# Optimization experiments

Measured on AMD Instinct MI355X. Metric: run time of the kernel, lower is better.

Reference implementation:

```python
import jax, jax.numpy as jnp
import numpy as np


def setup_inputs() -> dict:
    key = jax.random.key(0)
    k1, k2, k3, k4 = jax.random.split(key, 4)
    N, C_in, C_out, H, W, K = 32, 128, 256, 56, 56, 3
    x = jax.random.normal(k1, (N, C_in, H, W), dtype=jnp.float32)
    # ternary weights in {-1, 0, +1}, stored as int8 like the torch buffer
    w_q = jax.random.randint(k2, (C_out, C_in, K, K), -1, 2).astype(jnp.int8)
    s = jax.random.uniform(k3, (C_out, 1, 1), dtype=jnp.float32) + 0.5
    bias = jax.random.normal(k4, (C_out,), dtype=jnp.float32)
    return {"x": x, "w_q": w_q, "s": s, "bias": bias}


def reference(x, w_q, s, bias):
    # y = conv2d(x, w_q.float()) * s + bias, stride=1, padding=1, dilation=1, groups=1
    w = w_q.astype(x.dtype)  # ternary {-1,0,+1} cast to float, as in torch
    y = jax.lax.conv_general_dilated(
        x, w,
        window_strides=(1, 1),
        padding=((1, 1), (1, 1)),
        lhs_dilation=(1, 1),
        rhs_dilation=(1, 1),
        dimension_numbers=("NCHW", "OIHW", "NCHW"),
        feature_group_count=1,
    )
    y = y * s  # s: [C_out,1,1] broadcasts over [N,C_out,H,W]
    y = y + bias.reshape(1, -1, 1, 1)
    return y
```

## Files before the change

kernel.cpp:

```cpp
#include <hip/hip_runtime.h>
#include <hip/hip_bf16.h>

typedef unsigned short ushort_t;

#define N_IMG 32
#define C_IN  128
#define C_OUT 256
#define H_SZ  56
#define W_SZ  56
#define HW_SZ (H_SZ * W_SZ)
#define K_TOT (C_IN * 9)
#define SP_TOT (N_IMG * HW_SZ)

typedef __attribute__((ext_vector_type(8))) short bf16x8;
typedef __attribute__((ext_vector_type(4))) float floatx4;

__device__ __forceinline__ void gl_lds16(const ushort_t* g, ushort_t* l) {
  __builtin_amdgcn_global_load_lds(
      (const __attribute__((address_space(1))) void*)g,
      (__attribute__((address_space(3))) void*)l, 16, 0, 0);
}

__device__ __forceinline__ ushort_t f2bf(float f) {
  __hip_bfloat16 b = __float2bfloat16(f);
  return *reinterpret_cast<ushort_t*>(&b);
}

__global__ void wtrans_kernel(const int* __restrict__ wq, ushort_t* __restrict__ wt,
                              ushort_t* __restrict__ zeros) {
  int tid = threadIdx.x;
  if (blockIdx.x == 0 && tid < 128) zeros[tid] = 0;
  int idx = blockIdx.x * 256 + tid;
  if (idx >= C_OUT * K_TOT) return;
  int co = idx / K_TOT;
  int k  = idx - co * K_TOT;
  int tap = k >> 7;
  int c   = k & 127;
  int kh = tap / 3, kw = tap - kh * 3;
  int v = wq[((co * C_IN + c) * 3 + kh) * 3 + kw];
  wt[idx] = f2bf((float)v);
}

#define LDT 69
__global__ __launch_bounds__(256) void xtrans_kernel(const float* __restrict__ x,
                                                     ushort_t* __restrict__ xt) {
  __shared__ float tile[64 * LDT];
  int b = blockIdx.x;
  int n = b / 98;
  int r = b - n * 98;
  int cg = r / 49;
  int hwg = r - cg * 49;
  int hw0 = hwg * 64, c0 = cg * 64;
  int t = threadIdx.x;
  int cl = t >> 4;
  int f4 = t & 15;
  const float* xb = x + ((size_t)(n * C_IN + c0) * HW_SZ + hw0);
#pragma unroll
  for (int p = 0; p < 4; ++p) {
    int c = p * 16 + cl;
    float4 v = *(const float4*)(xb + (size_t)c * HW_SZ + f4 * 4);
    float* dst = &tile[c * LDT + f4 * 4];
    dst[0] = v.x; dst[1] = v.y; dst[2] = v.z; dst[3] = v.w;
  }
  __syncthreads();
  int cp  = t & 31;
  int hwl = t >> 5;
  ushort_t* ob = xt + (size_t)(n * HW_SZ + hw0) * C_IN + c0;
#pragma unroll
  for (int p = 0; p < 8; ++p) {
    int hw = p * 8 + hwl;
    unsigned int u = (unsigned int)f2bf(tile[(2 * cp) * LDT + hw]) |
                     ((unsigned int)f2bf(tile[(2 * cp + 1) * LDT + hw]) << 16);
    *(unsigned int*)&ob[(size_t)hw * C_IN + 2 * cp] = u;
  }
}

__global__ __launch_bounds__(256) void bitconv_kernel(
    const ushort_t* __restrict__ wt, const ushort_t* __restrict__ xt,
    const ushort_t* __restrict__ zeros,
    const float* __restrict__ s, const float* __restrict__ bias,
    float* __restrict__ out) {
  __shared__ ushort_t As[128 * 64];
  __shared__ ushort_t Bs[128 * 64];

  int d = blockIdx.x;
  int sp_idx = (d >> 4) * 8 + (d & 7);
  int co0 = ((d >> 3) & 1) * 128;
  int sp0 = sp_idx * 128;

  int tid  = threadIdx.x;
  int lane = tid & 63;
  int wid  = tid >> 6;
  int l15  = lane & 15;
  int quad = lane >> 4;
  int lrow8 = lane >> 3;
  int lk8   = (lane & 7) * 8;
  int wave_m = (wid >> 1) * 64;
  int wave_n = (wid & 1) * 64;

  const ushort_t* a_src0 = wt + (size_t)(co0 + wid * 32 + lrow8) * K_TOT + lk8;
  int bh[4], bw[4];
  const ushort_t* b_img[4];
#pragma unroll
  for (int j = 0; j < 4; ++j) {
    int sp   = sp0 + wid * 32 + j * 8 + lrow8;
    int nimg = sp / HW_SZ;
    int rem  = sp - nimg * HW_SZ;
    bh[j] = rem / W_SZ;
    bw[j] = rem - bh[j] * W_SZ;
    b_img[j] = xt + (size_t)nimg * HW_SZ * C_IN;
  }

  floatx4 acc[4][4];
#pragma unroll
  for (int mi = 0; mi < 4; ++mi)
#pragma unroll
    for (int ni = 0; ni < 4; ++ni)
      acc[mi][ni] = (floatx4){0.f, 0.f, 0.f, 0.f};

  for (int tap = 0; tap < 9; ++tap) {
    int dh = tap / 3 - 1;
    int dw = tap - (dh + 1) * 3 - 1;
    const ushort_t* bsrc[4];
#pragma unroll
    for (int j = 0; j < 4; ++j) {
      int hh2 = bh[j] + dh, ww2 = bw[j] + dw;
      bool valid = (hh2 >= 0) & (hh2 < H_SZ) & (ww2 >= 0) & (ww2 < W_SZ);
      bsrc[j] = valid ? (b_img[j] + (size_t)(hh2 * W_SZ + ww2) * C_IN + lk8)
                      : (zeros + lk8);
    }
    int ktap = tap * C_IN;
#pragma unroll
    for (int c0 = 0; c0 < C_IN; c0 += 64) {
#pragma unroll
      for (int j = 0; j < 4; ++j) {
        gl_lds16(a_src0 + (size_t)j * 8 * K_TOT + ktap + c0,
                 &As[(wid * 32 + j * 8) * 64]);
        gl_lds16(bsrc[j] + c0, &Bs[(wid * 32 + j * 8) * 64]);
      }
      __syncthreads();
#pragma unroll
      for (int ksub = 0; ksub < 2; ++ksub) {
        bf16x8 af[4], bfv[4];
#pragma unroll
        for (int mi = 0; mi < 4; ++mi)
          af[mi] = *(const bf16x8*)&As[(wave_m + mi * 16 + l15) * 64 +
                                       ksub * 32 + quad * 8];
#pragma unroll
        for (int ni = 0; ni < 4; ++ni)
          bfv[ni] = *(const bf16x8*)&Bs[(wave_n + ni * 16 + l15) * 64 +
                                        ksub * 32 + quad * 8];
#pragma unroll
        for (int mi = 0; mi < 4; ++mi)
#pragma unroll
          for (int ni = 0; ni < 4; ++ni)
            acc[mi][ni] = __builtin_amdgcn_mfma_f32_16x16x32_bf16(
                af[mi], bfv[ni], acc[mi][ni], 0, 0, 0);
      }
      __syncthreads();
    }
  }

  int spl_[4], nimg_[4];
#pragma unroll
  for (int ni = 0; ni < 4; ++ni) {
    int sp = sp0 + wave_n + ni * 16 + l15;
    int nimg = sp / HW_SZ;
    nimg_[ni] = nimg;
    spl_[ni]  = sp - nimg * HW_SZ;
  }
#pragma unroll
  for (int mi = 0; mi < 4; ++mi) {
#pragma unroll
    for (int r = 0; r < 4; ++r) {
      int co = co0 + wave_m + mi * 16 + quad * 4 + r;
      float sv = s[co];
      float bv = bias[co];
#pragma unroll
      for (int ni = 0; ni < 4; ++ni) {
        out[((size_t)nimg_[ni] * C_OUT + co) * HW_SZ + spl_[ni]] =
            acc[mi][ni][r] * sv + bv;
      }
    }
  }
}

extern "C" void kernel_launch(void* const* d_in, const int* in_sizes, int n_in,
                              void* d_out, int out_size, void* d_ws, size_t ws_size,
                              hipStream_t stream) {
  const float* x    = (const float*)d_in[0];
  const int*   wq   = (const int*)d_in[1];
  const float* s    = (const float*)d_in[2];
  const float* bias = (const float*)d_in[3];
  float* out = (float*)d_out;

  char* ws = (char*)d_ws;
  ushort_t* zeros = (ushort_t*)ws;
  ushort_t* wt    = (ushort_t*)(ws + 256);
  ushort_t* xt    = (ushort_t*)(ws + 590080);

  hipLaunchKernelGGL(wtrans_kernel, dim3((C_OUT * K_TOT) / 256), dim3(256), 0, stream,
                     wq, wt, zeros);
  hipLaunchKernelGGL(xtrans_kernel, dim3(N_IMG * 98), dim3(256), 0, stream, x, xt);
  hipLaunchKernelGGL(bitconv_kernel, dim3((C_OUT / 128) * (SP_TOT / 128)), dim3(256),
                     0, stream, wt, xt, zeros, s, bias, out);
}
```

Baseline: 239.8 us.

## Load MFMA fragments directly from global memory, dropping LDS staging

Removes the shared-memory tiles and async global-to-LDS copies, so each wave loads its A and B bf16x8 fragments straight from global memory into registers, with the tap loop fully unrolled. This drops the __syncthreads barriers and the LDS round trip. In exchange, data that was shared between the two waves along each dimension is now fetched twice through the cache. Exposed global-load latency is also no longer hidden by block-wide staging, and the full unroll raises register pressure.

```diff
diff --git a/kernel.cpp b/kernel.cpp
--- a/kernel.cpp
+++ b/kernel.cpp
@@ -14,12 +14,6 @@
 
 typedef __attribute__((ext_vector_type(8))) short bf16x8;
 typedef __attribute__((ext_vector_type(4))) float floatx4;
-
-__device__ __forceinline__ void gl_lds16(const ushort_t* g, ushort_t* l) {
-  __builtin_amdgcn_global_load_lds(
-      (const __attribute__((address_space(1))) void*)g,
-      (__attribute__((address_space(3))) void*)l, 16, 0, 0);
-}
 
 __device__ __forceinline__ ushort_t f2bf(float f) {
   __hip_bfloat16 b = __float2bfloat16(f);
@@ -80,9 +74,6 @@
     const ushort_t* __restrict__ zeros,
     const float* __restrict__ s, const float* __restrict__ bias,
     float* __restrict__ out) {
-  __shared__ ushort_t As[128 * 64];
-  __shared__ ushort_t Bs[128 * 64];
-
   int d = blockIdx.x;
   int sp_idx = (d >> 4) * 8 + (d & 7);
   int co0 = ((d >> 3) & 1) * 128;
@@ -93,22 +84,24 @@
   int wid  = tid >> 6;
   int l15  = lane & 15;
   int quad = lane >> 4;
-  int lrow8 = lane >> 3;
-  int lk8   = (lane & 7) * 8;
   int wave_m = (wid >> 1) * 64;
   int wave_n = (wid & 1) * 64;
 
-  const ushort_t* a_src0 = wt + (size_t)(co0 + wid * 32 + lrow8) * K_TOT + lk8;
+  const ushort_t* a_base[4];
+#pragma unroll
+  for (int mi = 0; mi < 4; ++mi)
+    a_base[mi] = wt + (size_t)(co0 + wave_m + mi * 16 + l15) * K_TOT + quad * 8;
+
   int bh[4], bw[4];
   const ushort_t* b_img[4];
 #pragma unroll
-  for (int j = 0; j < 4; ++j) {
-    int sp   = sp0 + wid * 32 + j * 8 + lrow8;
+  for (int ni = 0; ni < 4; ++ni) {
+    int sp   = sp0 + wave_n + ni * 16 + l15;
     int nimg = sp / HW_SZ;
     int rem  = sp - nimg * HW_SZ;
-    bh[j] = rem / W_SZ;
-    bw[j] = rem - bh[j] * W_SZ;
-    b_img[j] = xt + (size_t)nimg * HW_SZ * C_IN;
+    bh[ni] = rem / W_SZ;
+    bw[ni] = rem - bh[ni] * W_SZ;
+    b_img[ni] = xt + (size_t)nimg * HW_SZ * C_IN;
   }
 
   floatx4 acc[4][4];
@@ -118,46 +111,34 @@
     for (int ni = 0; ni < 4; ++ni)
       acc[mi][ni] = (floatx4){0.f, 0.f, 0.f, 0.f};
 
+#pragma unroll
   for (int tap = 0; tap < 9; ++tap) {
-    int dh = tap / 3 - 1;
-    int dw = tap - (dh + 1) * 3 - 1;
-    const ushort_t* bsrc[4];
+    const int dh = tap / 3 - 1;
+    const int dw = tap % 3 - 1;
+    const ushort_t* bptr[4];
 #pragma unroll
-    for (int j = 0; j < 4; ++j) {
-      int hh2 = bh[j] + dh, ww2 = bw[j] + dw;
+    for (int ni = 0; ni < 4; ++ni) {
+      int hh2 = bh[ni] + dh, ww2 = bw[ni] + dw;
       bool valid = (hh2 >= 0) & (hh2 < H_SZ) & (ww2 >= 0) & (ww2 < W_SZ);
-      bsrc[j] = valid ? (b_img[j] + (size_t)(hh2 * W_SZ + ww2) * C_IN + lk8)
-                      : (zeros + lk8);
+      bptr[ni] = valid ? (b_img[ni] + (size_t)(hh2 * W_SZ + ww2) * C_IN + quad * 8)
+                       : (zeros + quad * 8);
     }
-    int ktap = tap * C_IN;
 #pragma unroll
-    for (int c0 = 0; c0 < C_IN; c0 += 64) {
+    for (int ksub = 0; ksub < 4; ++ksub) {
+      const int k0 = tap * C_IN + ksub * 32;
+      bf16x8 af[4], bfv[4];
 #pragma unroll
-      for (int j = 0; j < 4; ++j) {
-        gl_lds16(a_src0 + (size_t)j * 8 * K_TOT + ktap + c0,
-                 &As[(wid * 32 + j * 8) * 64]);
-        gl_lds16(bsrc[j] + c0, &Bs[(wid * 32 + j * 8) * 64]);
-      }
-      __syncthreads();
+      for (int mi = 0; mi < 4; ++mi)
+        af[mi] = *(const bf16x8*)(a_base[mi] + k0);
 #pragma unroll
-      for (int ksub = 0; ksub < 2; ++ksub) {
-        bf16x8 af[4], bfv[4];
+      for (int ni = 0; ni < 4; ++ni)
+        bfv[ni] = *(const bf16x8*)(bptr[ni] + ksub * 32);
 #pragma unroll
-        for (int mi = 0; mi < 4; ++mi)
-          af[mi] = *(const bf16x8*)&As[(wave_m + mi * 16 + l15) * 64 +
-                                       ksub * 32 + quad * 8];
+      for (int mi = 0; mi < 4; ++mi)
 #pragma unroll
         for (int ni = 0; ni < 4; ++ni)
-          bfv[ni] = *(const bf16x8*)&Bs[(wave_n + ni * 16 + l15) * 64 +
-                                        ksub * 32 + quad * 8];
-#pragma unroll
-        for (int mi = 0; mi < 4; ++mi)
-#pragma unroll
-          for (int ni = 0; ni < 4; ++ni)
-            acc[mi][ni] = __builtin_amdgcn_mfma_f32_16x16x32_bf16(
-                af[mi], bfv[ni], acc[mi][ni], 0, 0, 0);
-      }
-      __syncthreads();
+          acc[mi][ni] = __builtin_amdgcn_mfma_f32_16x16x32_bf16(
+              af[mi], bfv[ni], acc[mi][ni], 0, 0, 0);
     }
   }
 
```

Result: slower. 362.6 us (+51.2%).
